# Optimization experiments

Hardware: AMD Instinct MI355X
Metric: run time of the kernel (lower is better)

## Reference

```python
import jax, jax.numpy as jnp
import numpy as np

B, IN, K, E = 2048, 1024, 128, 64  # batch, in_features, n_concepts, emb_size


def setup_inputs() -> dict:
    key = jax.random.key(0)
    k1, k2, k3, k4, k5 = jax.random.split(key, 5)
    x = jax.random.normal(k1, (B, IN), dtype=jnp.float32)
    # stacked per-concept Linear(in_features, 2*emb_size)
    W = jax.random.normal(k2, (K, IN, 2 * E), dtype=jnp.float32) * (1.0 / np.sqrt(IN))
    b = jax.random.normal(k3, (K, 2 * E), dtype=jnp.float32) * 0.01
    # shared prob predictor Linear(2*emb_size, 1)
    wp = jax.random.normal(k4, (2 * E,), dtype=jnp.float32) * (1.0 / np.sqrt(2 * E))
    bp = jax.random.normal(k5, (), dtype=jnp.float32) * 0.01
    return {"x": x, "W": W, "b": b, "wp": wp, "bp": bp}


def reference(x, W, b, wp, bp):
    # batched GEMM over all concepts at once: [B,K,2E]
    context = jax.nn.leaky_relu(jnp.einsum('bi,kio->bko', x, W) + b)
    # shared predictor + sigmoid: [B,K]
    c_pred = jax.nn.sigmoid(jnp.einsum('bko,o->bk', context, wp) + bp)
    ctx_pos = context[..., :E]
    ctx_neg = context[..., E:]
    p = c_pred[..., None]
    c_emb = ctx_pos * p + ctx_neg * (1.0 - p)  # [B,K,E]
    return c_emb, c_pred
```

## Files before the change

kernel.cpp:

```cpp
#include <hip/hip_runtime.h>

typedef unsigned int u32;
typedef unsigned short u16;
typedef __attribute__((ext_vector_type(8))) __bf16 bf16x8;
typedef __attribute__((ext_vector_type(4))) float f32x4;

#define B_SZ 2048
#define IN_SZ 1024
#define K_SZ 128
#define E_SZ 64
#define TWOE 128
#define BK 32
static const size_t OUT_EMB = (size_t)B_SZ * K_SZ * E_SZ;

__device__ __forceinline__ u16 f2bf(float f) {
    u32 u = __builtin_bit_cast(u32, f);
    u32 r = u + 0x7fffu + ((u >> 16) & 1u);
    return (u16)(r >> 16);
}

__device__ __forceinline__ void async16(const void* g, void* l) {
    __builtin_amdgcn_global_load_lds((const __attribute__((address_space(1))) u32*)g,
                                     (__attribute__((address_space(3))) u32*)l, 16, 0, 0);
}

__global__ void __launch_bounds__(256) cvt_x(const float* __restrict__ in, u16* __restrict__ outp, int n4) {
    int i = blockIdx.x * blockDim.x + threadIdx.x;
    if (i < n4) {
        float4 v = ((const float4*)in)[i];
        u32 lo = (u32)f2bf(v.x) | ((u32)f2bf(v.y) << 16);
        u32 hi = (u32)f2bf(v.z) | ((u32)f2bf(v.w) << 16);
        ((uint2*)outp)[i] = make_uint2(lo, hi);
    }
}

__global__ void __launch_bounds__(256) cvt_w(const float* __restrict__ W, u16* __restrict__ wt) {
    __shared__ u16 tr[128][72];
    const int k = blockIdx.y, i0 = blockIdx.x * 64;
    const float* src = W + (size_t)k * IN_SZ * TWOE + (size_t)i0 * TWOE;
#pragma unroll
    for (int r = 0; r < 8; ++r) {
        int idx = r * 256 + threadIdx.x;
        int i = idx >> 5;
        int o = (idx & 31) * 4;
        float4 v = ((const float4*)src)[idx];
        tr[o + 0][i] = f2bf(v.x);
        tr[o + 1][i] = f2bf(v.y);
        tr[o + 2][i] = f2bf(v.z);
        tr[o + 3][i] = f2bf(v.w);
    }
    __syncthreads();
    const int o = threadIdx.x >> 1, h = threadIdx.x & 1;
    u16* dst = wt + ((size_t)(k * TWOE + o) * IN_SZ) + i0 + h * 32;
#pragma unroll
    for (int s = 0; s < 4; ++s) {
        uint4 v = *(const uint4*)&tr[o][h * 32 + s * 8];
        ((uint4*)dst)[s] = v;
    }
}

__global__ void __launch_bounds__(256) cvt_pred(const float* __restrict__ pw, float* __restrict__ out) {
    __shared__ float t[128][132];
    const int b0 = blockIdx.x * 128;
    const int tid = threadIdx.x;
#pragma unroll
    for (int i = 0; i < 16; ++i) {
        int idx = i * 256 + tid;
        int kk = idx >> 5, c4 = (idx & 31) * 4;
        float4 v = *(const float4*)(pw + (size_t)kk * B_SZ + b0 + c4);
        t[kk][c4 + 0] = v.x; t[kk][c4 + 1] = v.y; t[kk][c4 + 2] = v.z; t[kk][c4 + 3] = v.w;
    }
    __syncthreads();
#pragma unroll
    for (int i = 0; i < 16; ++i) {
        int idx = i * 256 + tid;
        int bl = idx >> 5, k4 = (idx & 31) * 4;
        float4 v = make_float4(t[k4 + 0][bl], t[k4 + 1][bl], t[k4 + 2][bl], t[k4 + 3][bl]);
        *(float4*)(out + OUT_EMB + (size_t)(b0 + bl) * K_SZ + k4) = v;
    }
}

__global__ void __launch_bounds__(256, 2) fused_main(
    const u16* __restrict__ xb,
    const u16* __restrict__ wt,
    const float* __restrict__ bias, const float* __restrict__ wpv,
    const float* __restrict__ bpp, float* __restrict__ out,
    float* __restrict__ pw) {
    __shared__ union {
        u16 stage[3][12288];
        struct { float pl[256][2]; float ex[256][65]; } epi;
    } sm;

    const int tid = threadIdx.x;
    const int l = tid & 63, w = tid >> 6;
    const int wm = w >> 1, wn = w & 1;
    const int hi = l >> 4, lo16 = l & 15;
    const int q = l >> 2, sl = l & 3;

    const int id = blockIdx.x;
    const int xcd = id & 7, j2 = id >> 3;
    const int k = (xcd << 4) | (j2 >> 3);
    const int brow = (j2 & 7) << 8;

    const u16* abase = xb + (size_t)(brow + w * 16 + q) * IN_SZ + (sl ^ ((q >> 1) & 3)) * 8;
    const u16* bbase = wt + ((size_t)k * TWOE + w * 16 + q) * IN_SZ + (sl ^ ((q >> 1) & 3)) * 8;

    const int xsl = (hi ^ ((lo16 >> 1) & 3)) << 4;
    const int aoff = (wm * 128 + lo16) * 64 + xsl;
    const int boff = 16384 + (wn * 64 + lo16) * 64 + xsl;

    f32x4 acc[8][4] = {};

    auto STAGE = [&](int bi, int tt) {
        const int koff = tt * BK;
        u16* sbuf = &sm.stage[bi][0];
#pragma unroll
        for (int i = 0; i < 4; ++i)
            async16(abase + (size_t)i * 64 * IN_SZ + koff, sbuf + i * 2048 + w * 512);
#pragma unroll
        for (int jj = 0; jj < 2; ++jj)
            async16(bbase + (size_t)jj * 64 * IN_SZ + koff, sbuf + 8192 + jj * 2048 + w * 512);
    };

    const float bp_val = *bpp;
    float bvals[4], wvals[4];
#pragma unroll
    for (int n = 0; n < 4; ++n) {
        const int o = wn * 64 + n * 16 + lo16;
        bvals[n] = bias[k * TWOE + o];
        wvals[n] = wpv[o];
    }

    STAGE(0, 0);
    STAGE(1, 1);
    asm volatile("s_waitcnt vmcnt(6)" ::: "memory");
    __builtin_amdgcn_s_barrier();

    for (int t = 0; t < 32; ++t) {
        const int b0 = t % 3;
        if (t < 30) STAGE((b0 + 2) % 3, t + 2);
        const char* base = (const char*)&sm.stage[b0][0];
        bf16x8 af[8], bfr[4];
#pragma unroll
        for (int m = 0; m < 8; ++m)
            af[m] = *(const bf16x8*)(base + aoff + m * 1024);
#pragma unroll
        for (int n = 0; n < 4; ++n)
            bfr[n] = *(const bf16x8*)(base + boff + n * 1024);
        __builtin_amdgcn_s_setprio(1);
#pragma unroll
        for (int m = 0; m < 8; ++m)
#pragma unroll
            for (int n = 0; n < 4; ++n)
                acc[m][n] = __builtin_amdgcn_mfma_f32_16x16x32_bf16(af[m], bfr[n], acc[m][n], 0, 0, 0);
        __builtin_amdgcn_s_setprio(0);
        if (t < 30) asm volatile("s_waitcnt vmcnt(6) lgkmcnt(0)" ::: "memory");
        else        asm volatile("s_waitcnt vmcnt(0) lgkmcnt(0)" ::: "memory");
        __builtin_amdgcn_s_barrier();
    }

    float p[8][4];
#pragma unroll
    for (int m = 0; m < 8; ++m)
#pragma unroll
        for (int j = 0; j < 4; ++j) {
            float s = 0.f;
#pragma unroll
            for (int n = 0; n < 4; ++n) {
                float v = acc[m][n][j] + bvals[n];
                v = v > 0.f ? v : 0.01f * v;
                acc[m][n][j] = v;
                s += v * wvals[n];
            }
            s += __shfl_xor(s, 1);
            s += __shfl_xor(s, 2);
            s += __shfl_xor(s, 4);
            s += __shfl_xor(s, 8);
            p[m][j] = s;
        }
    if (lo16 == 0) {
#pragma unroll
        for (int m = 0; m < 8; ++m)
#pragma unroll
            for (int j = 0; j < 4; ++j)
                sm.epi.pl[wm * 128 + m * 16 + hi * 4 + j][wn] = p[m][j];
    }
    __builtin_amdgcn_s_barrier();
#pragma unroll
    for (int m = 0; m < 8; ++m)
#pragma unroll
        for (int j = 0; j < 4; ++j) {
            const int rg = wm * 128 + m * 16 + hi * 4 + j;
            const float z = sm.epi.pl[rg][0] + sm.epi.pl[rg][1] + bp_val;
            p[m][j] = 1.f / (1.f + __expf(-z));
        }
    if (wn == 0 && lo16 == 0) {
        if (pw) {
#pragma unroll
            for (int m = 0; m < 8; ++m) {
                float4 v = make_float4(p[m][0], p[m][1], p[m][2], p[m][3]);
                *(float4*)(pw + (size_t)k * B_SZ + brow + wm * 128 + m * 16 + hi * 4) = v;
            }
        } else {
#pragma unroll
            for (int m = 0; m < 8; ++m)
#pragma unroll
                for (int j = 0; j < 4; ++j) {
                    const int b = brow + wm * 128 + m * 16 + hi * 4 + j;
                    out[OUT_EMB + (size_t)b * K_SZ + k] = p[m][j];
                }
        }
    }
    if (wn == 1) {
#pragma unroll
        for (int m = 0; m < 8; ++m)
#pragma unroll
            for (int n = 0; n < 4; ++n)
#pragma unroll
                for (int j = 0; j < 4; ++j)
                    sm.epi.ex[wm * 128 + m * 16 + hi * 4 + j][n * 16 + lo16] =
                        (1.f - p[m][j]) * acc[m][n][j];
    }
    __builtin_amdgcn_s_barrier();
    if (wn == 0) {
#pragma unroll
        for (int m = 0; m < 8; ++m)
#pragma unroll
            for (int n = 0; n < 4; ++n)
#pragma unroll
                for (int j = 0; j < 4; ++j) {
                    const int rl = wm * 128 + m * 16 + hi * 4 + j;
                    const int b = brow + rl;
                    const int e = n * 16 + lo16;
                    out[((size_t)b * K_SZ + k) * E_SZ + e] =
                        p[m][j] * acc[m][n][j] + sm.epi.ex[rl][e];
                }
    }
}

__global__ void __launch_bounds__(128) fallback_kernel(
    const float* __restrict__ x, const float* __restrict__ W,
    const float* __restrict__ bias, const float* __restrict__ wpv,
    const float* __restrict__ bpp, float* __restrict__ out) {
    const int k = blockIdx.y;
    const int b0 = blockIdx.x * 8;
    const int o = threadIdx.x;
    __shared__ float xs[8][1024];
    __shared__ float red[2];
    __shared__ float exch[64];
    for (int idx = threadIdx.x; idx < 8 * 1024; idx += 128)
        xs[idx >> 10][idx & 1023] = x[(size_t)(b0 + (idx >> 10)) * IN_SZ + (idx & 1023)];
    __syncthreads();
    float a[8] = {};
    for (int i = 0; i < 1024; ++i) {
        float wv = W[((size_t)k * IN_SZ + i) * TWOE + o];
#pragma unroll
        for (int bb = 0; bb < 8; ++bb) a[bb] += xs[bb][i] * wv;
    }
    const float bo = bias[k * TWOE + o], wo = wpv[o], bpv = *bpp;
    for (int bb = 0; bb < 8; ++bb) {
        float c = a[bb] + bo;
        c = c > 0.f ? c : 0.01f * c;
        float s = c * wo;
        for (int off = 1; off < 64; off <<= 1) s += __shfl_xor(s, off);
        if ((threadIdx.x & 63) == 0) red[threadIdx.x >> 6] = s;
        __syncthreads();
        float p = 1.f / (1.f + expf(-(red[0] + red[1] + bpv)));
        if (o >= 64) exch[o - 64] = (1.f - p) * c;
        __syncthreads();
        if (o < 64) out[((size_t)(b0 + bb) * K_SZ + k) * E_SZ + o] = p * c + exch[o];
        if (o == 0) out[OUT_EMB + (size_t)(b0 + bb) * K_SZ + k] = p;
        __syncthreads();
    }
}

extern "C" void kernel_launch(void* const* d_in, const int* in_sizes, int n_in,
                              void* d_out, int out_size, void* d_ws, size_t ws_size,
                              hipStream_t stream) {
    const float* x = (const float*)d_in[0];
    const float* W = (const float*)d_in[1];
    const float* bias = (const float*)d_in[2];
    const float* wp = (const float*)d_in[3];
    const float* bp = (const float*)d_in[4];
    float* out = (float*)d_out;

    const size_t X_ELEMS = (size_t)B_SZ * IN_SZ;
    const size_t WT_ELEMS = (size_t)K_SZ * TWOE * IN_SZ;
    const size_t PW_ELEMS = (size_t)K_SZ * B_SZ;
    const size_t NEED_BASE = (X_ELEMS + WT_ELEMS) * sizeof(u16);
    const size_t NEED_FULL = NEED_BASE + PW_ELEMS * sizeof(float);

    if (ws_size >= NEED_BASE) {
        u16* xb = (u16*)d_ws;
        u16* wt = xb + X_ELEMS;
        float* pw = (ws_size >= NEED_FULL) ? (float*)(wt + WT_ELEMS) : nullptr;
        int n4 = (int)(X_ELEMS / 4);
        cvt_x<<<dim3((n4 + 255) / 256), 256, 0, stream>>>(x, xb, n4);
        cvt_w<<<dim3(16, 128), 256, 0, stream>>>(W, wt);
        fused_main<<<dim3(1024), 256, 0, stream>>>(xb, wt, bias, wp, bp, out, pw);
        if (pw) cvt_pred<<<dim3(16), 256, 0, stream>>>(pw, out);
    } else {
        fallback_kernel<<<dim3(B_SZ / 8, K_SZ), 128, 0, stream>>>(x, W, bias, wp, bp, out);
    }
}
```

Before: 119.8 us.

## Use 256x256 tiles with 8 waves and a finer-grained double-buffered pipeline

The fused GEMM kernel now runs 512-thread blocks that each compute two concepts (256 output columns) over 256 batch rows, halving the grid and reusing each A tile across both concepts. The K loop uses a BK of 64, split into two 32-wide halves and double-buffered, and global-to-LDS staging is interleaved into eight phases per step with a barrier around each MFMA group. The epilogue is adapted to keep per-concept reduction and exchange buffers. LDS use grows to 128KB per block and there are more barriers per iteration, which may limit occupancy and add synchronisation cost.

```diff
diff --git a/kernel.cpp b/kernel.cpp
--- a/kernel.cpp
+++ b/kernel.cpp
@@ -10,7 +10,6 @@
 #define K_SZ 128
 #define E_SZ 64
 #define TWOE 128
-#define BK 32
 static const size_t OUT_EMB = (size_t)B_SZ * K_SZ * E_SZ;
 
 __device__ __forceinline__ u16 f2bf(float f) {
@@ -80,160 +79,190 @@
     }
 }
 
-__global__ void __launch_bounds__(256, 2) fused_main(
+__global__ void __launch_bounds__(512, 2) fused_main(
     const u16* __restrict__ xb,
     const u16* __restrict__ wt,
     const float* __restrict__ bias, const float* __restrict__ wpv,
     const float* __restrict__ bpp, float* __restrict__ out,
     float* __restrict__ pw) {
     __shared__ union {
-        u16 stage[3][12288];
-        struct { float pl[256][2]; float ex[256][65]; } epi;
+        u16 stage[65536];
+        struct { float pl[2][256][2]; float ex[2][256][66]; } epi;
     } sm;
+    char* smb = (char*)&sm;
 
     const int tid = threadIdx.x;
     const int l = tid & 63, w = tid >> 6;
-    const int wm = w >> 1, wn = w & 1;
+    const int wm = w >> 2, wn = w & 3;
     const int hi = l >> 4, lo16 = l & 15;
-    const int q = l >> 2, sl = l & 3;
+    const int q = l >> 2;
+    const int swz = (l & 3) ^ ((l >> 3) & 3);
 
     const int id = blockIdx.x;
-    const int xcd = id & 7, j2 = id >> 3;
-    const int k = (xcd << 4) | (j2 >> 3);
-    const int brow = (j2 & 7) << 8;
-
-    const u16* abase = xb + (size_t)(brow + w * 16 + q) * IN_SZ + (sl ^ ((q >> 1) & 3)) * 8;
-    const u16* bbase = wt + ((size_t)k * TWOE + w * 16 + q) * IN_SZ + (sl ^ ((q >> 1) & 3)) * 8;
+    const int xcd = id & 7, j = id >> 3;
+    const int kp = (xcd << 3) | (j >> 3);
+    const int brow = (j & 7) << 8;
+
+    const u16* abase = xb + (size_t)(brow + w * 16 + q) * IN_SZ + swz * 8;
+    const u16* bbase = wt + ((size_t)kp * 256 + w * 16 + q) * IN_SZ + swz * 8;
 
     const int xsl = (hi ^ ((lo16 >> 1) & 3)) << 4;
-    const int aoff = (wm * 128 + lo16) * 64 + xsl;
-    const int boff = 16384 + (wn * 64 + lo16) * 64 + xsl;
 
     f32x4 acc[8][4] = {};
-
-    auto STAGE = [&](int bi, int tt) {
-        const int koff = tt * BK;
-        u16* sbuf = &sm.stage[bi][0];
-#pragma unroll
-        for (int i = 0; i < 4; ++i)
-            async16(abase + (size_t)i * 64 * IN_SZ + koff, sbuf + i * 2048 + w * 512);
-#pragma unroll
-        for (int jj = 0; jj < 2; ++jj)
-            async16(bbase + (size_t)jj * 64 * IN_SZ + koff, sbuf + 8192 + jj * 2048 + w * 512);
+    bf16x8 bfr[4];
+
+    auto SA = [&](int d, int kh, int t) {
+        u16* dst = (u16*)&sm + (d * 2 + kh) * 8192 + w * 512;
+        const u16* src = abase + t * 64 + kh * 32;
+        async16(src, dst);
+        async16(src + (size_t)128 * IN_SZ, dst + 4096);
     };
-
+    auto SB = [&](int d, int kh, int t) {
+        u16* dst = (u16*)&sm + 32768 + (d * 2 + kh) * 8192 + w * 512;
+        const u16* src = bbase + t * 64 + kh * 32;
+        async16(src, dst);
+        async16(src + (size_t)128 * IN_SZ, dst + 4096);
+    };
+
+#define VM4 asm volatile("s_waitcnt vmcnt(4)" ::: "memory")
+#define VM0 asm volatile("s_waitcnt vmcnt(0)" ::: "memory")
+#define NOPX ((void)0)
+#define PHASE(D, KH, HALF, STG, VM)                                              \
+    {                                                                            \
+        bf16x8 af[4];                                                            \
+        if ((HALF) == 0) {                                                       \
+            const char* rb = smb + 65536 + ((D) * 2 + (KH)) * 16384;             \
+            _Pragma("unroll") for (int n = 0; n < 4; ++n)                        \
+                bfr[n] = *(const bf16x8*)(rb + (wn * 64 + n * 16 + lo16) * 64 + xsl); \
+        }                                                                        \
+        {                                                                        \
+            const char* ra = smb + ((D) * 2 + (KH)) * 16384;                     \
+            _Pragma("unroll") for (int mm = 0; mm < 4; ++mm)                     \
+                af[mm] = *(const bf16x8*)(ra + (wm * 128 + ((HALF) * 4 + mm) * 16 + lo16) * 64 + xsl); \
+        }                                                                        \
+        STG;                                                                     \
+        __builtin_amdgcn_s_barrier();                                            \
+        asm volatile("s_waitcnt lgkmcnt(0)" ::: "memory");                       \
+        __builtin_amdgcn_s_setprio(1);                                           \
+        _Pragma("unroll") for (int mm = 0; mm < 4; ++mm)                         \
+            _Pragma("unroll") for (int n = 0; n < 4; ++n)                        \
+                acc[(HALF) * 4 + mm][n] = __builtin_amdgcn_mfma_f32_16x16x32_bf16( \
+                    af[mm], bfr[n], acc[(HALF) * 4 + mm][n], 0, 0, 0);           \
+        __builtin_amdgcn_s_setprio(0);                                           \
+        VM;                                                                      \
+        __builtin_amdgcn_s_barrier();                                            \
+    }
+
+    SA(0, 0, 0); SB(0, 0, 0); SA(0, 1, 0); SB(0, 1, 0);
+    VM4;
+    __builtin_amdgcn_s_barrier();
+
+#pragma unroll 1
+    for (int tt = 0; tt < 14; tt += 2) {
+        PHASE(0, 0, 0, SA(1, 0, tt + 1), NOPX);
+        PHASE(0, 0, 1, SB(1, 0, tt + 1), VM4);
+        PHASE(0, 1, 0, SA(1, 1, tt + 1), NOPX);
+        PHASE(0, 1, 1, SB(1, 1, tt + 1), VM4);
+        PHASE(1, 0, 0, SA(0, 0, tt + 2), NOPX);
+        PHASE(1, 0, 1, SB(0, 0, tt + 2), VM4);
+        PHASE(1, 1, 0, SA(0, 1, tt + 2), NOPX);
+        PHASE(1, 1, 1, SB(0, 1, tt + 2), VM4);
+    }
+    PHASE(0, 0, 0, SA(1, 0, 15), NOPX);
+    PHASE(0, 0, 1, SB(1, 0, 15), VM4);
+    PHASE(0, 1, 0, SA(1, 1, 15), NOPX);
+    PHASE(0, 1, 1, SB(1, 1, 15), VM4);
+    PHASE(1, 0, 0, NOPX, NOPX);
+    PHASE(1, 0, 1, NOPX, VM0);
+    PHASE(1, 1, 0, NOPX, NOPX);
+    PHASE(1, 1, 1, NOPX, VM0);
+#undef PHASE
+
+    const int ksel = wn >> 1, oh = wn & 1;
+    const int kglob = kp * 2 + ksel;
     const float bp_val = *bpp;
     float bvals[4], wvals[4];
 #pragma unroll
     for (int n = 0; n < 4; ++n) {
-        const int o = wn * 64 + n * 16 + lo16;
-        bvals[n] = bias[k * TWOE + o];
+        const int o = oh * 64 + n * 16 + lo16;
+        bvals[n] = bias[kglob * TWOE + o];
         wvals[n] = wpv[o];
     }
-
-    STAGE(0, 0);
-    STAGE(1, 1);
-    asm volatile("s_waitcnt vmcnt(6)" ::: "memory");
-    __builtin_amdgcn_s_barrier();
-
-    for (int t = 0; t < 32; ++t) {
-        const int b0 = t % 3;
-        if (t < 30) STAGE((b0 + 2) % 3, t + 2);
-        const char* base = (const char*)&sm.stage[b0][0];
-        bf16x8 af[8], bfr[4];
-#pragma unroll
-        for (int m = 0; m < 8; ++m)
-            af[m] = *(const bf16x8*)(base + aoff + m * 1024);
-#pragma unroll
-        for (int n = 0; n < 4; ++n)
-            bfr[n] = *(const bf16x8*)(base + boff + n * 1024);
-        __builtin_amdgcn_s_setprio(1);
-#pragma unroll
-        for (int m = 0; m < 8; ++m)
-#pragma unroll
-            for (int n = 0; n < 4; ++n)
-                acc[m][n] = __builtin_amdgcn_mfma_f32_16x16x32_bf16(af[m], bfr[n], acc[m][n], 0, 0, 0);
-        __builtin_amdgcn_s_setprio(0);
-        if (t < 30) asm volatile("s_waitcnt vmcnt(6) lgkmcnt(0)" ::: "memory");
-        else        asm volatile("s_waitcnt vmcnt(0) lgkmcnt(0)" ::: "memory");
-        __builtin_amdgcn_s_barrier();
-    }
-
     float p[8][4];
 #pragma unroll
     for (int m = 0; m < 8; ++m)
 #pragma unroll
-        for (int j = 0; j < 4; ++j) {
+        for (int jj = 0; jj < 4; ++jj) {
             float s = 0.f;
 #pragma unroll
             for (int n = 0; n < 4; ++n) {
-                float v = acc[m][n][j] + bvals[n];
+                float v = acc[m][n][jj] + bvals[n];
                 v = v > 0.f ? v : 0.01f * v;
-                acc[m][n][j] = v;
+                acc[m][n][jj] = v;
                 s += v * wvals[n];
             }
             s += __shfl_xor(s, 1);
             s += __shfl_xor(s, 2);
             s += __shfl_xor(s, 4);
             s += __shfl_xor(s, 8);
-            p[m][j] = s;
+            p[m][jj] = s;
         }
     if (lo16 == 0) {
 #pragma unroll
         for (int m = 0; m < 8; ++m)
 #pragma unroll
-            for (int j = 0; j < 4; ++j)
-                sm.epi.pl[wm * 128 + m * 16 + hi * 4 + j][wn] = p[m][j];
+            for (int jj = 0; jj < 4; ++jj)
+                sm.epi.pl[ksel][wm * 128 + m * 16 + hi * 4 + jj][oh] = p[m][jj];
     }
     __builtin_amdgcn_s_barrier();
 #pragma unroll
     for (int m = 0; m < 8; ++m)
 #pragma unroll
-        for (int j = 0; j < 4; ++j) {
-            const int rg = wm * 128 + m * 16 + hi * 4 + j;
-            const float z = sm.epi.pl[rg][0] + sm.epi.pl[rg][1] + bp_val;
-            p[m][j] = 1.f / (1.f + __expf(-z));
+        for (int jj = 0; jj < 4; ++jj) {
+            const int rg = wm * 128 + m * 16 + hi * 4 + jj;
+            const float z = sm.epi.pl[ksel][rg][0] + sm.epi.pl[ksel][rg][1] + bp_val;
+            p[m][jj] = 1.f / (1.f + __expf(-z));
         }
-    if (wn == 0 && lo16 == 0) {
+    if (oh == 0 && lo16 == 0) {
         if (pw) {
 #pragma unroll
             for (int m = 0; m < 8; ++m) {
                 float4 v = make_float4(p[m][0], p[m][1], p[m][2], p[m][3]);
-                *(float4*)(pw + (size_t)k * B_SZ + brow + wm * 128 + m * 16 + hi * 4) = v;
+                *(float4*)(pw + (size_t)kglob * B_SZ + brow + wm * 128 + m * 16 + hi * 4) = v;
             }
         } else {
 #pragma unroll
             for (int m = 0; m < 8; ++m)
 #pragma unroll
-                for (int j = 0; j < 4; ++j) {
-                    const int b = brow + wm * 128 + m * 16 + hi * 4 + j;
-                    out[OUT_EMB + (size_t)b * K_SZ + k] = p[m][j];
+                for (int jj = 0; jj < 4; ++jj) {
+                    const int b = brow + wm * 128 + m * 16 + hi * 4 + jj;
+                    out[OUT_EMB + (size_t)b * K_SZ + kglob] = p[m][jj];
                 }
         }
     }
-    if (wn == 1) {
+    if (oh == 1) {
 #pragma unroll
         for (int m = 0; m < 8; ++m)
 #pragma unroll
             for (int n = 0; n < 4; ++n)
 #pragma unroll
-                for (int j = 0; j < 4; ++j)
-                    sm.epi.ex[wm * 128 + m * 16 + hi * 4 + j][n * 16 + lo16] =
-                        (1.f - p[m][j]) * acc[m][n][j];
+                for (int jj = 0; jj < 4; ++jj)
+                    sm.epi.ex[ksel][wm * 128 + m * 16 + hi * 4 + jj][n * 16 + lo16] =
+                        (1.f - p[m][jj]) * acc[m][n][jj];
     }
     __builtin_amdgcn_s_barrier();
-    if (wn == 0) {
+    if (oh == 0) {
 #pragma unroll
         for (int m = 0; m < 8; ++m)
 #pragma unroll
             for (int n = 0; n < 4; ++n)
 #pragma unroll
-                for (int j = 0; j < 4; ++j) {
-                    const int rl = wm * 128 + m * 16 + hi * 4 + j;
+                for (int jj = 0; jj < 4; ++jj) {
+                    const int rl = wm * 128 + m * 16 + hi * 4 + jj;
                     const int b = brow + rl;
                     const int e = n * 16 + lo16;
-                    out[((size_t)b * K_SZ + k) * E_SZ + e] =
-                        p[m][j] * acc[m][n][j] + sm.epi.ex[rl][e];
+                    out[((size_t)b * K_SZ + kglob) * E_SZ + e] =
+                        p[m][jj] * acc[m][n][jj] + sm.epi.ex[ksel][rl][e];
                 }
     }
 }
@@ -297,7 +326,7 @@
         int n4 = (int)(X_ELEMS / 4);
         cvt_x<<<dim3((n4 + 255) / 256), 256, 0, stream>>>(x, xb, n4);
         cvt_w<<<dim3(16, 128), 256, 0, stream>>>(W, wt);
-        fused_main<<<dim3(1024), 256, 0, stream>>>(xb, wt, bias, wp, bp, out, pw);
+        fused_main<<<dim3(512), 512, 0, stream>>>(xb, wt, bias, wp, bp, out, pw);
         if (pw) cvt_pred<<<dim3(16), 256, 0, stream>>>(pw, out);
     } else {
         fallback_kernel<<<dim3(B_SZ / 8, K_SZ), 128, 0, stream>>>(x, W, bias, wp, bp, out);
```

Result: faster. 114.9 us (-4.1%).
